# Kernel optimization log

Measured on AMD Instinct MI355X. Metric: run time of the kernel, lower is better.

## Reference

```python
import jax, jax.numpy as jnp
import numpy as np

D = 256      # embedding_dim
DI = 512     # inner dim = proj_factor * D
H = 4        # num heads
DH = DI // H # head dim
L = 4        # num blocks
K = 4        # causal conv kernel size

def _ln(x, g, b):
    mu = jnp.mean(x, -1, keepdims=True)
    v = jnp.var(x, -1, keepdims=True)
    return (x - mu) * jax.lax.rsqrt(v + 1e-5) * g + b

def _causal_conv(x, w, b):
    # x [B,S,DI], w [K,DI] depthwise causal conv
    S = x.shape[1]
    xp = jnp.pad(x, ((0, 0), (K - 1, 0), (0, 0)))
    out = b
    for j in range(K):
        out = out + xp[:, j:j + S, :] * w[j]
    return out

def _mlstm(q, k, v, ip, fp):
    # parallel stabilized mLSTM. q,k,v [B,S,H,DH]; ip,fp [B,S,H]
    q = q.transpose(0, 2, 1, 3)
    k = k.transpose(0, 2, 1, 3)
    v = v.transpose(0, 2, 1, 3)
    ip = ip.transpose(0, 2, 1)  # [B,H,S]
    fp = fp.transpose(0, 2, 1)
    lf = jax.nn.log_sigmoid(fp)                      # log forget gates
    Fc = jnp.cumsum(lf, axis=-1)
    Fc = jnp.concatenate([jnp.zeros_like(Fc[..., :1]), Fc], axis=-1)  # [B,H,S+1]
    logfg = Fc[..., 1:, None] - Fc[..., None, 1:]    # [B,H,S,S]: sum of log f over (s,t]
    S_len = q.shape[2]
    tri = jnp.tril(jnp.ones((S_len, S_len), dtype=bool))
    logD = jnp.where(tri, logfg + ip[..., None, :], jnp.float32(-1e30))
    m = jnp.max(logD, axis=-1, keepdims=True)        # stabilizer
    Dm = jnp.exp(logD - m)
    qk = jnp.einsum('bhtd,bhsd->bhts', q, k) * (DH ** -0.5)
    C = qk * Dm
    norm = jnp.maximum(jnp.abs(jnp.sum(C, axis=-1, keepdims=True)), jnp.exp(-m))
    h = jnp.einsum('bhts,bhsd->bhtd', C / (norm + 1e-6), v)
    return h.transpose(0, 2, 1, 3)

def _forward(x, time_features, Wp, bp, ln_g, ln_b, Wup, bup, conv_w, conv_b,
             Wq, Wk, Wv, Wif, bif, gn_g, gn_b, skip, Wdown, bdown,
             lnf_g, lnf_b, Wf, bf):
    B, S = x.shape
    xi = jnp.concatenate([x[..., None], time_features], axis=-1)  # [B,S,5]
    h = xi @ Wp + bp                                              # [B,S,D]
    for l in range(L):
        res = h
        hn = _ln(h, ln_g[l], ln_b[l])
        up = hn @ Wup[l] + bup[l]                 # [B,S,2*DI]
        xm, z = up[..., :DI], up[..., DI:]
        xc = jax.nn.silu(_causal_conv(xm, conv_w[l], conv_b[l]))
        q = (xc @ Wq[l]).reshape(B, S, H, DH)
        k = (xc @ Wk[l]).reshape(B, S, H, DH)
        v = (xm @ Wv[l]).reshape(B, S, H, DH)
        gi = jnp.concatenate([q.reshape(B, S, DI), k.reshape(B, S, DI), v.reshape(B, S, DI)], axis=-1)
        gates = gi @ Wif[l] + bif[l]              # [B,S,2H]
        ht = _mlstm(q, k, v, gates[..., :H], gates[..., H:])  # [B,S,H,DH]
        ht = _ln(ht, gn_g[l].reshape(H, DH), gn_b[l].reshape(H, DH)).reshape(B, S, DI)
        ht = ht + skip[l] * xc
        ht = ht * jax.nn.silu(z)
        h = res + ht @ Wdown[l] + bdown[l]
    h = _ln(h, lnf_g, lnf_b)
    return h[:, -1, :] @ Wf + bf                  # [B,1]

def setup_inputs():
    key = jax.random.key(0)
    ks = jax.random.split(key, 16)
    B, S = 8, 1024
    sd = jnp.float32(0.02)
    return {
        'x': jax.random.normal(ks[0], (B, S), jnp.float32),
        'time_features': jax.random.normal(ks[1], (B, S, 4), jnp.float32),
        'Wp': jax.random.normal(ks[2], (5, D)) * sd, 'bp': jnp.zeros((D,)),
        'ln_g': jnp.ones((L, D)), 'ln_b': jnp.zeros((L, D)),
        'Wup': jax.random.normal(ks[3], (L, D, 2 * DI)) * sd, 'bup': jnp.zeros((L, 2 * DI)),
        'conv_w': jax.random.normal(ks[4], (L, K, DI)) * sd, 'conv_b': jnp.zeros((L, DI)),
        'Wq': jax.random.normal(ks[5], (L, DI, DI)) * sd,
        'Wk': jax.random.normal(ks[6], (L, DI, DI)) * sd,
        'Wv': jax.random.normal(ks[7], (L, DI, DI)) * sd,
        'Wif': jax.random.normal(ks[8], (L, 3 * DI, 2 * H)) * sd, 'bif': jnp.zeros((L, 2 * H)),
        'gn_g': jnp.ones((L, DI)), 'gn_b': jnp.zeros((L, DI)),
        'skip': jnp.ones((L, DI)),
        'Wdown': jax.random.normal(ks[9], (L, DI, D)) * sd, 'bdown': jnp.zeros((L, D)),
        'lnf_g': jnp.ones((D,)), 'lnf_b': jnp.zeros((D,)),
        'Wf': jax.random.normal(ks[10], (D, 1)) * sd, 'bf': jnp.zeros((1,)),
    }

def reference(x, time_features, Wp, bp, ln_g, ln_b, Wup, bup, conv_w, conv_b,
              Wq, Wk, Wv, Wif, bif, gn_g, gn_b, skip, Wdown, bdown,
              lnf_g, lnf_b, Wf, bf):
    return _forward(x, time_features, Wp, bp, ln_g, ln_b, Wup, bup, conv_w, conv_b,
                    Wq, Wk, Wv, Wif, bif, gn_g, gn_b, skip, Wdown, bdown,
                    lnf_g, lnf_b, Wf, bf)
```

## Files before the change

### kernel.cpp

```cpp
#include <hip/hip_runtime.h>
#include <hip/hip_bf16.h>
#include <math.h>

#define S 1024
#define NLAYER 4

typedef __bf16 bf16x8 __attribute__((ext_vector_type(8)));
typedef float floatx4 __attribute__((ext_vector_type(4)));

__device__ __forceinline__ float wave_sum(float v) {
  #pragma unroll
  for (int off = 32; off > 0; off >>= 1) v += __shfl_xor(v, off, 64);
  return v;
}

__global__ __launch_bounds__(256) void embed_kernel(
    const float* __restrict__ x, const float* __restrict__ tf,
    const float* __restrict__ Wp, const float* __restrict__ bp,
    const float* __restrict__ g, const float* __restrict__ b,
    float* __restrict__ h, __bf16* __restrict__ hn) {
  int row = blockIdx.x;
  int n = threadIdx.x;
  float xv = x[row];
  const float* t4 = tf + (size_t)row * 4;
  float acc = bp[n] + xv * Wp[n];
  acc += t4[0] * Wp[256 + n];
  acc += t4[1] * Wp[512 + n];
  acc += t4[2] * Wp[768 + n];
  acc += t4[3] * Wp[1024 + n];
  h[(size_t)row * 256 + n] = acc;
  __shared__ float red[4];
  int wid = n >> 6, lane = n & 63;
  float s = wave_sum(acc);
  if (lane == 0) red[wid] = s;
  __syncthreads();
  float mu = (red[0] + red[1] + red[2] + red[3]) * (1.f / 256.f);
  __syncthreads();
  float d = acc - mu;
  float s2 = wave_sum(d * d);
  if (lane == 0) red[wid] = s2;
  __syncthreads();
  float var = (red[0] + red[1] + red[2] + red[3]) * (1.f / 256.f);
  float rs = rsqrtf(var + 1e-5f);
  hn[(size_t)row * 256 + n] = (__bf16)(d * rs * g[n] + b[n]);
}

__global__ __launch_bounds__(256) void wtrans_kernel(
    const float* __restrict__ Wup, const float* __restrict__ Wq,
    const float* __restrict__ Wk, const float* __restrict__ Wv,
    const float* __restrict__ Wdown,
    __bf16* __restrict__ WupT, __bf16* __restrict__ WqkT,
    __bf16* __restrict__ WvT, __bf16* __restrict__ WdownT) {
  __shared__ float T[32][33];
  int bid = blockIdx.x;
  int layer = bid / 1152, rr = bid % 1152;
  const float* src; __bf16* dst; int K, N, tile;
  if (rr < 256)       { src = Wup   + layer * 262144; dst = WupT  + layer * 262144;          K = 256; N = 1024; tile = rr; }
  else if (rr < 512)  { src = Wq    + layer * 262144; dst = WqkT  + layer * 524288;          K = 512; N = 512;  tile = rr - 256; }
  else if (rr < 768)  { src = Wk    + layer * 262144; dst = WqkT  + layer * 524288 + 262144; K = 512; N = 512;  tile = rr - 512; }
  else if (rr < 1024) { src = Wv    + layer * 262144; dst = WvT   + layer * 262144;          K = 512; N = 512;  tile = rr - 768; }
  else                { src = Wdown + layer * 131072; dst = WdownT + layer * 131072;         K = 512; N = 256;  tile = rr - 1024; }
  int ntn = N >> 5;
  int tk = tile / ntn, tn = tile % ntn;
  int tid = threadIdx.x;
  int r = tid >> 3, c4 = (tid & 7) * 4;
  float4 v = *(const float4*)(src + (size_t)(tk * 32 + r) * N + tn * 32 + c4);
  T[c4 + 0][r] = v.x; T[c4 + 1][r] = v.y; T[c4 + 2][r] = v.z; T[c4 + 3][r] = v.w;
  __syncthreads();
  __bf16 o[4];
  #pragma unroll
  for (int j = 0; j < 4; ++j) o[j] = (__bf16)T[r][c4 + j];
  *(uint2*)(dst + (size_t)(tn * 32 + r) * K + tk * 32 + c4) = *(uint2*)o;
}

__global__ __launch_bounds__(256) void wgprep_kernel(
    const float* __restrict__ Wq, const float* __restrict__ Wk,
    const float* __restrict__ Wv, const float* __restrict__ Wif,
    float* __restrict__ wg) {
  int bid = blockIdx.x;
  int l = bid >> 8;
  int rem = bid & 255;
  int sel = rem >> 7;
  int kg = rem & 127;
  int tid = threadIdx.x;
  int wv = tid >> 6, lane = tid & 63;
  int k = kg * 4 + wv;
  const float* wif = Wif + (size_t)l * 1536 * 8;
  float part[8] = {0, 0, 0, 0, 0, 0, 0, 0};
  if (sel == 0) {
    const float* qr = Wq + (size_t)l * 262144 + (size_t)k * 512;
    const float* kr = Wk + (size_t)l * 262144 + (size_t)k * 512;
    #pragma unroll
    for (int i = 0; i < 8; ++i) {
      int n = lane + i * 64;
      float qv = qr[n], kv = kr[n];
      const float* wq8 = wif + (size_t)n * 8;
      const float* wk8 = wif + (size_t)(512 + n) * 8;
      #pragma unroll
      for (int j = 0; j < 8; ++j) part[j] += qv * wq8[j] + kv * wk8[j];
    }
  } else {
    const float* vr = Wv + (size_t)l * 262144 + (size_t)k * 512;
    #pragma unroll
    for (int i = 0; i < 8; ++i) {
      int n = lane + i * 64;
      float vv = vr[n];
      const float* wv8 = wif + (size_t)(1024 + n) * 8;
      #pragma unroll
      for (int j = 0; j < 8; ++j) part[j] += vv * wv8[j];
    }
  }
  #pragma unroll
  for (int j = 0; j < 8; ++j) part[j] = wave_sum(part[j]);
  if (lane < 8) wg[(size_t)l * 8192 + sel * 4096 + (size_t)k * 8 + lane] = part[lane];
}

__global__ __launch_bounds__(256) void ln256_kernel(
    const float* __restrict__ x, const float* __restrict__ g,
    const float* __restrict__ b, __bf16* __restrict__ y) {
  int row = blockIdx.x, tid = threadIdx.x;
  __shared__ float red[4];
  float v = x[(size_t)row * 256 + tid];
  float s = wave_sum(v);
  int wid = tid >> 6, lane = tid & 63;
  if (lane == 0) red[wid] = s;
  __syncthreads();
  float mu = (red[0] + red[1] + red[2] + red[3]) * (1.f / 256.f);
  __syncthreads();
  float d = v - mu;
  float s2 = wave_sum(d * d);
  if (lane == 0) red[wid] = s2;
  __syncthreads();
  float var = (red[0] + red[1] + red[2] + red[3]) * (1.f / 256.f);
  float rs = rsqrtf(var + 1e-5f);
  y[(size_t)row * 256 + tid] = (__bf16)(d * rs * g[tid] + b[tid]);
}

template <int MODE, int ACC>
__global__ __launch_bounds__(256) void hgemm(
    const __bf16* __restrict__ A, int lda,
    const __bf16* __restrict__ BT, int Kdim,
    const float* __restrict__ bias,
    void* __restrict__ Cout, int ldc) {
  __shared__ __bf16 As[128][40];
  __shared__ __bf16 Bs[128][40];
  int tid = threadIdx.x;
  int bm = blockIdx.x * 128, bn = blockIdx.y * 128;
  int wid = tid >> 6, lane = tid & 63;
  int wr = wid >> 1, wc = wid & 1;
  int lg = lane >> 4, li = lane & 15;
  floatx4 acc[4][4];
  #pragma unroll
  for (int i = 0; i < 4; ++i)
    #pragma unroll
    for (int j = 0; j < 4; ++j) acc[i][j] = (floatx4)(0.f);

  int arow = tid >> 2, aseg = tid & 3;
  bf16x8 pa0, pa1, pb0, pb1;
  auto pre = [&](int k0) {
    pa0 = *(const bf16x8*)(A + (size_t)(bm + arow) * lda + k0 + aseg * 8);
    pa1 = *(const bf16x8*)(A + (size_t)(bm + arow + 64) * lda + k0 + aseg * 8);
    pb0 = *(const bf16x8*)(BT + (size_t)(bn + arow) * Kdim + k0 + aseg * 8);
    pb1 = *(const bf16x8*)(BT + (size_t)(bn + arow + 64) * Kdim + k0 + aseg * 8);
  };
  pre(0);
  for (int k0 = 0; k0 < Kdim; k0 += 32) {
    __syncthreads();
    *(bf16x8*)&As[arow][aseg * 8] = pa0;
    *(bf16x8*)&As[arow + 64][aseg * 8] = pa1;
    *(bf16x8*)&Bs[arow][aseg * 8] = pb0;
    *(bf16x8*)&Bs[arow + 64][aseg * 8] = pb1;
    __syncthreads();
    if (k0 + 32 < Kdim) pre(k0 + 32);
    bf16x8 af[4], bfr[4];
    #pragma unroll
    for (int mi = 0; mi < 4; ++mi)
      af[mi] = *(const bf16x8*)&As[wr * 64 + mi * 16 + li][lg * 8];
    #pragma unroll
    for (int ni = 0; ni < 4; ++ni)
      bfr[ni] = *(const bf16x8*)&Bs[wc * 64 + ni * 16 + li][lg * 8];
    #pragma unroll
    for (int mi = 0; mi < 4; ++mi)
      #pragma unroll
      for (int ni = 0; ni < 4; ++ni)
        acc[mi][ni] = __builtin_amdgcn_mfma_f32_16x16x32_bf16(af[mi], bfr[ni], acc[mi][ni], 0, 0, 0);
  }
  if (MODE == 1) {
    __bf16* eb = &As[0][0];
    const int PITCH = 136;
    __bf16* C = (__bf16*)Cout;
    #pragma unroll
    for (int mi = 0; mi < 4; ++mi) {
      __syncthreads();
      #pragma unroll
      for (int ni = 0; ni < 4; ++ni) {
        int col = wc * 64 + ni * 16 + li;
        float bz = bias ? bias[bn + col] : 0.f;
        #pragma unroll
        for (int r = 0; r < 4; ++r) {
          int lr = wr * 16 + lg * 4 + r;
          eb[lr * PITCH + col] = (__bf16)(acc[mi][ni][r] + bz);
        }
      }
      __syncthreads();
      #pragma unroll
      for (int i = 0; i < 2; ++i) {
        int lr = (tid >> 4) + i * 16;
        int c8 = (tid & 15) * 8;
        bf16x8 v = *(const bf16x8*)&eb[lr * PITCH + c8];
        int row_g = bm + (lr >> 4) * 64 + mi * 16 + (lr & 15);
        *(bf16x8*)(C + (size_t)row_g * ldc + bn + c8) = v;
      }
    }
  } else {
    #pragma unroll
    for (int mi = 0; mi < 4; ++mi) {
      int row = bm + wr * 64 + mi * 16 + lg * 4;
      #pragma unroll
      for (int ni = 0; ni < 4; ++ni) {
        int col = bn + wc * 64 + ni * 16 + li;
        if (MODE == 2) {
          __bf16 o4[4];
          #pragma unroll
          for (int r = 0; r < 4; ++r) o4[r] = (__bf16)acc[mi][ni][r];
          __bf16* vt = (__bf16*)Cout;
          size_t off = ((size_t)((row >> 10) * 4 + (col >> 7)) * 128 + (col & 127)) * 1024 + (row & 1023);
          *(uint2*)(vt + off) = *(uint2*)o4;
        } else {
          float bz = bias ? bias[col] : 0.f;
          float* C = (float*)Cout;
          #pragma unroll
          for (int r = 0; r < 4; ++r) {
            float v = acc[mi][ni][r] + bz;
            if (ACC) v += C[(size_t)(row + r) * ldc + col];
            C[(size_t)(row + r) * ldc + col] = v;
          }
        }
      }
    }
  }
}

__global__ __launch_bounds__(256) void conv_silu_kernel(
    const __bf16* __restrict__ up, const float* __restrict__ cw,
    const float* __restrict__ cb, const float* __restrict__ wg,
    const float* __restrict__ bif, __bf16* __restrict__ xc,
    float* __restrict__ gates) {
  int tid = threadIdx.x;
  int wv = tid >> 6, lane = tid & 63;
  int row = blockIdx.x * 4 + wv;
  int c8 = lane * 8;
  int t = row & (S - 1);
  float acc[8];
  *(float4*)&acc[0] = *(const float4*)(cb + c8);
  *(float4*)&acc[4] = *(const float4*)(cb + c8 + 4);
  float xm[8];
  #pragma unroll
  for (int j = 0; j < 4; ++j) {
    int tt = t - 3 + j;
    if (tt >= 0) {
      bf16x8 xv = *(const bf16x8*)(up + (size_t)(row - 3 + j) * 1024 + c8);
      float4 w0 = *(const float4*)(cw + j * 512 + c8);
      float4 w1 = *(const float4*)(cw + j * 512 + c8 + 4);
      acc[0] += w0.x * (float)xv[0]; acc[1] += w0.y * (float)xv[1];
      acc[2] += w0.z * (float)xv[2]; acc[3] += w0.w * (float)xv[3];
      acc[4] += w1.x * (float)xv[4]; acc[5] += w1.y * (float)xv[5];
      acc[6] += w1.z * (float)xv[6]; acc[7] += w1.w * (float)xv[7];
      if (j == 3) {
        #pragma unroll
        for (int m = 0; m < 8; ++m) xm[m] = (float)xv[m];
      }
    }
  }
  bf16x8 o;
  float xcs[8];
  #pragma unroll
  for (int m = 0; m < 8; ++m) {
    float sg = 1.f / (1.f + __expf(-acc[m]));
    xcs[m] = acc[m] * sg;
    o[m] = (__bf16)xcs[m];
  }
  *(bf16x8*)(xc + (size_t)row * 512 + c8) = o;
  const float* w1 = wg + (size_t)c8 * 8;
  const float* w2 = wg + 4096 + (size_t)c8 * 8;
  float part[8] = {0, 0, 0, 0, 0, 0, 0, 0};
  #pragma unroll
  for (int m = 0; m < 8; ++m) {
    const float* a = w1 + m * 8;
    const float* b = w2 + m * 8;
    #pragma unroll
    for (int j = 0; j < 8; ++j) part[j] += xcs[m] * a[j] + xm[m] * b[j];
  }
  #pragma unroll
  for (int j = 0; j < 8; ++j) part[j] = wave_sum(part[j]);
  if (lane < 8) gates[(size_t)row * 8 + lane] = part[lane] + bif[lane];
}

__global__ __launch_bounds__(64) void scan_kernel(
    const float* __restrict__ gates, float* __restrict__ gout,
    float* __restrict__ Mout, float* __restrict__ NFout) {
  int bh = blockIdx.x;
  int bb = bh >> 2, hh = bh & 3;
  int lane = threadIdx.x;
  float ip[16], pf[16];
  #pragma unroll
  for (int i = 0; i < 16; ++i) {
    int t = lane * 16 + i;
    const float* grow = gates + ((size_t)(bb * S + t)) * 8;
    ip[i] = grow[hh];
    float fp = grow[4 + hh];
    float lf = fminf(fp, 0.f) - log1pf(__expf(-fabsf(fp)));
    pf[i] = (i == 0) ? lf : pf[i - 1] + lf;
  }
  float T = pf[15];
  float inc = T;
  #pragma unroll
  for (int off = 1; off < 64; off <<= 1) {
    float v = __shfl_up(inc, off, 64);
    if (lane >= off) inc += v;
  }
  float excl = inc - T;
  float F[16], g[16], pm[16];
  #pragma unroll
  for (int i = 0; i < 16; ++i) {
    F[i] = excl + pf[i];
    g[i] = ip[i] - F[i];
    pm[i] = (i == 0) ? g[0] : fmaxf(pm[i - 1], g[i]);
  }
  float Mx = pm[15];
  float incm = Mx;
  #pragma unroll
  for (int off = 1; off < 64; off <<= 1) {
    float v = __shfl_up(incm, off, 64);
    if (lane >= off) incm = fmaxf(incm, v);
  }
  float em = __shfl_up(incm, 1, 64);
  if (lane == 0) em = -3.4e38f;
  #pragma unroll
  for (int i = 0; i < 16; ++i) {
    int t = lane * 16 + i;
    size_t o = (size_t)bh * S + t;
    float M = fmaxf(em, pm[i]);
    gout[o] = g[i];
    Mout[o] = M;
    NFout[o] = __expf(-F[i] - M);
  }
}

__global__ __launch_bounds__(256, 1) void attn_kernel(
    const __bf16* __restrict__ qk, const __bf16* __restrict__ vT,
    const float* __restrict__ gbuf, const float* __restrict__ Mbuf,
    const float* __restrict__ NFbuf,
    const float* __restrict__ gn_g, const float* __restrict__ gn_b,
    const float* __restrict__ skip,
    const __bf16* __restrict__ xc, const __bf16* __restrict__ up,
    __bf16* __restrict__ hd) {
  __shared__ __bf16 Ks[64][136];
  __shared__ __bf16 Vs[128][72];
  __shared__ __bf16 plds[4][2][16][72];
  __shared__ float gls[64];
  __shared__ float glds[128], blds[128], slds[128];
  int px = blockIdx.y, bh = blockIdx.x;
  int tqA = px, tqB = 15 - px;
  int bb = bh >> 2, hh = bh & 3;
  int tid = threadIdx.x;
  int wv = tid >> 6, lane = tid & 63;
  int lg = lane >> 4, li = lane & 15;
  int tbA = tqA * 64 + wv * 16;
  int tbB = tqB * 64 + wv * 16;
  const float scale = 0.08838834764831845f;

  if (tid < 128) {
    glds[tid] = gn_g[hh * 128 + tid];
    blds[tid] = gn_b[hh * 128 + tid];
    slds[tid] = skip[hh * 128 + tid];
  }

  bf16x8 aqA[4], aqB[4];
  {
    const __bf16* qpA = qk + ((size_t)(bb * S + tbA + li)) * 1024 + hh * 128 + lg * 8;
    const __bf16* qpB = qk + ((size_t)(bb * S + tbB + li)) * 1024 + hh * 128 + lg * 8;
    #pragma unroll
    for (int cd = 0; cd < 4; ++cd) {
      aqA[cd] = *(const bf16x8*)(qpA + cd * 32);
      aqB[cd] = *(const bf16x8*)(qpB + cd * 32);
    }
  }
  float mlA[4], nfA[4], mlB[4], nfB[4];
  #pragma unroll
  for (int r = 0; r < 4; ++r) {
    mlA[r] = Mbuf[(size_t)bh * S + tbA + lg * 4 + r];
    nfA[r] = NFbuf[(size_t)bh * S + tbA + lg * 4 + r];
    mlB[r] = Mbuf[(size_t)bh * S + tbB + lg * 4 + r];
    nfB[r] = NFbuf[(size_t)bh * S + tbB + lg * 4 + r];
  }

  floatx4 oA[8], oB[8];
  #pragma unroll
  for (int df = 0; df < 8; ++df) { oA[df] = (floatx4)(0.f); oB[df] = (floatx4)(0.f); }
  float rsA[4] = {0, 0, 0, 0}, rsB[4] = {0, 0, 0, 0};

  int krow = tid >> 3, kcol = tid & 7;
  bf16x8 kreg[4], vreg[4];
  float greg = 0.f;
  auto preload = [&](int st) {
    int s0 = st * 64;
    const __bf16* kp = qk + ((size_t)(bb * S + s0 + krow)) * 1024 + 512 + hh * 128;
    kreg[0] = *(const bf16x8*)(kp + kcol * 8);
    kreg[1] = *(const bf16x8*)(kp + (size_t)32 * 1024 + kcol * 8);
    kreg[2] = *(const bf16x8*)(kp + 64 + kcol * 8);
    kreg[3] = *(const bf16x8*)(kp + (size_t)32 * 1024 + 64 + kcol * 8);
    #pragma unroll
    for (int i = 0; i < 4; ++i)
      vreg[i] = *(const bf16x8*)(vT + ((size_t)(bh * 128 + krow + i * 32)) * 1024 + s0 + kcol * 8);
    if (tid < 64) greg = gbuf[(size_t)bh * S + s0 + tid];
  };
  preload(0);

  for (int st = 0; st <= tqB; ++st) {
    __syncthreads();
    *(bf16x8*)&Ks[krow][kcol * 8] = kreg[0];
    *(bf16x8*)&Ks[krow + 32][kcol * 8] = kreg[1];
    *(bf16x8*)&Ks[krow][64 + kcol * 8] = kreg[2];
    *(bf16x8*)&Ks[krow + 32][64 + kcol * 8] = kreg[3];
    #pragma unroll
    for (int i = 0; i < 4; ++i) *(bf16x8*)&Vs[krow + i * 32][kcol * 8] = vreg[i];
    if (tid < 64) gls[tid] = greg;
    __syncthreads();
    if (st < tqB) preload(st + 1);

    int s0 = st * 64;
    bool actA = (st <= tqA);
    #pragma unroll
    for (int ns = 0; ns < 4; ++ns) {
      bf16x8 bk0 = *(const bf16x8*)&Ks[ns * 16 + li][lg * 8];
      bf16x8 bk1 = *(const bf16x8*)&Ks[ns * 16 + li][32 + lg * 8];
      bf16x8 bk2 = *(const bf16x8*)&Ks[ns * 16 + li][64 + lg * 8];
      bf16x8 bk3 = *(const bf16x8*)&Ks[ns * 16 + li][96 + lg * 8];
      int s = s0 + ns * 16 + li;
      float gv = gls[ns * 16 + li];
      if (actA) {
        floatx4 pa = (floatx4)(0.f);
        pa = __builtin_amdgcn_mfma_f32_16x16x32_bf16(aqA[0], bk0, pa, 0, 0, 0);
        pa = __builtin_amdgcn_mfma_f32_16x16x32_bf16(aqA[1], bk1, pa, 0, 0, 0);
        pa = __builtin_amdgcn_mfma_f32_16x16x32_bf16(aqA[2], bk2, pa, 0, 0, 0);
        pa = __builtin_amdgcn_mfma_f32_16x16x32_bf16(aqA[3], bk3, pa, 0, 0, 0);
        #pragma unroll
        for (int r = 0; r < 4; ++r) {
          int t = tbA + lg * 4 + r;
          float val = pa[r] * scale * __expf(gv - mlA[r]);
          float w = (s <= t) ? val : 0.f;
          rsA[r] += w;
          plds[wv][0][lg * 4 + r][ns * 16 + li] = (__bf16)w;
        }
      }
      {
        floatx4 pb = (floatx4)(0.f);
        pb = __builtin_amdgcn_mfma_f32_16x16x32_bf16(aqB[0], bk0, pb, 0, 0, 0);
        pb = __builtin_amdgcn_mfma_f32_16x16x32_bf16(aqB[1], bk1, pb, 0, 0, 0);
        pb = __builtin_amdgcn_mfma_f32_16x16x32_bf16(aqB[2], bk2, pb, 0, 0, 0);
        pb = __builtin_amdgcn_mfma_f32_16x16x32_bf16(aqB[3], bk3, pb, 0, 0, 0);
        #pragma unroll
        for (int r = 0; r < 4; ++r) {
          int t = tbB + lg * 4 + r;
          float val = pb[r] * scale * __expf(gv - mlB[r]);
          float w = (s <= t) ? val : 0.f;
          rsB[r] += w;
          plds[wv][1][lg * 4 + r][ns * 16 + li] = (__bf16)w;
        }
      }
    }
    bf16x8 apA0, apA1, apB0, apB1;
    if (actA) {
      apA0 = *(const bf16x8*)&plds[wv][0][li][lg * 8];
      apA1 = *(const bf16x8*)&plds[wv][0][li][32 + lg * 8];
    }
    apB0 = *(const bf16x8*)&plds[wv][1][li][lg * 8];
    apB1 = *(const bf16x8*)&plds[wv][1][li][32 + lg * 8];
    #pragma unroll
    for (int df = 0; df < 8; ++df) {
      bf16x8 bv0 = *(const bf16x8*)&Vs[df * 16 + li][lg * 8];
      bf16x8 bv1 = *(const bf16x8*)&Vs[df * 16 + li][32 + lg * 8];
      if (actA) {
        oA[df] = __builtin_amdgcn_mfma_f32_16x16x32_bf16(apA0, bv0, oA[df], 0, 0, 0);
        oA[df] = __builtin_amdgcn_mfma_f32_16x16x32_bf16(apA1, bv1, oA[df], 0, 0, 0);
      }
      oB[df] = __builtin_amdgcn_mfma_f32_16x16x32_bf16(apB0, bv0, oB[df], 0, 0, 0);
      oB[df] = __builtin_amdgcn_mfma_f32_16x16x32_bf16(apB1, bv1, oB[df], 0, 0, 0);
    }
  }
  #pragma unroll
  for (int r = 0; r < 4; ++r) {
    float a = rsA[r], b = rsB[r];
    a += __shfl_xor(a, 1, 64); a += __shfl_xor(a, 2, 64);
    a += __shfl_xor(a, 4, 64); a += __shfl_xor(a, 8, 64);
    b += __shfl_xor(b, 1, 64); b += __shfl_xor(b, 2, 64);
    b += __shfl_xor(b, 4, 64); b += __shfl_xor(b, 8, 64);
    rsA[r] = a; rsB[r] = b;
  }
  #pragma unroll
  for (int tile = 0; tile < 2; ++tile) {
    int tb = tile == 0 ? tbA : tbB;
    #pragma unroll
    for (int r = 0; r < 4; ++r) {
      float rs = tile == 0 ? rsA[r] : rsB[r];
      float nf = tile == 0 ? nfA[r] : nfB[r];
      float inv = 1.f / (fmaxf(fabsf(rs), nf) + 1e-6f);
      float v8[8], s1 = 0.f, s2 = 0.f;
      #pragma unroll
      for (int df = 0; df < 8; ++df) {
        float v = (tile == 0 ? oA[df][r] : oB[df][r]) * inv;
        v8[df] = v;
        s1 += v;
        s2 += v * v;
      }
      s1 += __shfl_xor(s1, 1, 64); s1 += __shfl_xor(s1, 2, 64);
      s1 += __shfl_xor(s1, 4, 64); s1 += __shfl_xor(s1, 8, 64);
      s2 += __shfl_xor(s2, 1, 64); s2 += __shfl_xor(s2, 2, 64);
      s2 += __shfl_xor(s2, 4, 64); s2 += __shfl_xor(s2, 8, 64);
      float mu = s1 * (1.f / 128.f);
      float var = s2 * (1.f / 128.f) - mu * mu;
      float rq = rsqrtf(var + 1e-5f);
      int t = tb + lg * 4 + r;
      const __bf16* xr = xc + ((size_t)(bb * S + t)) * 512 + hh * 128 + li;
      const __bf16* zr = up + ((size_t)(bb * S + t)) * 1024 + 512 + hh * 128 + li;
      __bf16* od = hd + ((size_t)(bb * S + t)) * 512 + hh * 128 + li;
      #pragma unroll
      for (int df = 0; df < 8; ++df) {
        int c = df * 16 + li;
        float ln = (v8[df] - mu) * rq * glds[c] + blds[c];
        float val = ln + slds[c] * (float)xr[df * 16];
        float z = (float)zr[df * 16];
        float sg = 1.f / (1.f + __expf(-z));
        od[df * 16] = (__bf16)(val * (z * sg));
      }
    }
  }
}

__global__ __launch_bounds__(256) void final_kernel(
    const float* __restrict__ h, const float* __restrict__ g,
    const float* __restrict__ b, const float* __restrict__ Wf,
    const float* __restrict__ bf, float* __restrict__ out) {
  int bb = blockIdx.x, tid = threadIdx.x;
  size_t row = (size_t)(bb * S + S - 1) * 256;
  __shared__ float red[4];
  float v = h[row + tid];
  float s = wave_sum(v);
  int wid = tid >> 6, lane = tid & 63;
  if (lane == 0) red[wid] = s;
  __syncthreads();
  float mu = (red[0] + red[1] + red[2] + red[3]) * (1.f / 256.f);
  __syncthreads();
  float d = v - mu;
  float s2 = wave_sum(d * d);
  if (lane == 0) red[wid] = s2;
  __syncthreads();
  float var = (red[0] + red[1] + red[2] + red[3]) * (1.f / 256.f);
  float rs = rsqrtf(var + 1e-5f);
  float ln = d * rs * g[tid] + b[tid];
  float p = ln * Wf[tid];
  float psum = wave_sum(p);
  __syncthreads();
  if (lane == 0) red[wid] = psum;
  __syncthreads();
  if (tid == 0) out[bb] = red[0] + red[1] + red[2] + red[3] + bf[0];
}

extern "C" void kernel_launch(void* const* d_in, const int* in_sizes, int n_in,
                              void* d_out, int out_size, void* d_ws, size_t ws_size,
                              hipStream_t stream) {
  const float* x      = (const float*)d_in[0];
  const float* tf     = (const float*)d_in[1];
  const float* Wp     = (const float*)d_in[2];
  const float* bp     = (const float*)d_in[3];
  const float* ln_g   = (const float*)d_in[4];
  const float* ln_b   = (const float*)d_in[5];
  const float* Wup    = (const float*)d_in[6];
  const float* bup    = (const float*)d_in[7];
  const float* conv_w = (const float*)d_in[8];
  const float* conv_b = (const float*)d_in[9];
  const float* Wq     = (const float*)d_in[10];
  const float* Wk     = (const float*)d_in[11];
  const float* Wv     = (const float*)d_in[12];
  const float* Wif    = (const float*)d_in[13];
  const float* bif    = (const float*)d_in[14];
  const float* gn_g   = (const float*)d_in[15];
  const float* gn_b   = (const float*)d_in[16];
  const float* skip   = (const float*)d_in[17];
  const float* Wdown  = (const float*)d_in[18];
  const float* bdown  = (const float*)d_in[19];
  const float* lnf_g  = (const float*)d_in[20];
  const float* lnf_b  = (const float*)d_in[21];
  const float* Wf     = (const float*)d_in[22];
  const float* bf     = (const float*)d_in[23];
  float* out = (float*)d_out;

  float* h     = (float*)d_ws;
  float* gates = h + 2097152;
  float* gbuf  = gates + 65536;
  float* Mbuf  = gbuf + 32768;
  float* NFbuf = Mbuf + 32768;
  float* wgbuf = NFbuf + 32768;
  __bf16* hn   = (__bf16*)(wgbuf + 32768);
  __bf16* up   = hn + 2097152;
  __bf16* xc   = up + 8388608;
  __bf16* qk   = xc + 4194304;
  __bf16* vT   = qk + 8388608;
  __bf16* hd   = vT + 4194304;
  __bf16* WupT   = hd + 4194304;
  __bf16* WqkT   = WupT + 1048576;
  __bf16* WvT    = WqkT + 2097152;
  __bf16* WdownT = WvT + 1048576;

  wtrans_kernel<<<4608, 256, 0, stream>>>(Wup, Wq, Wk, Wv, Wdown,
                                          WupT, WqkT, WvT, WdownT);
  wgprep_kernel<<<1024, 256, 0, stream>>>(Wq, Wk, Wv, Wif, wgbuf);
  embed_kernel<<<8192, 256, 0, stream>>>(x, tf, Wp, bp, ln_g, ln_b, h, hn);
  for (int l = 0; l < NLAYER; ++l) {
    if (l > 0)
      ln256_kernel<<<8192, 256, 0, stream>>>(h, ln_g + l * 256, ln_b + l * 256, hn);
    hgemm<1, 0><<<dim3(64, 8), 256, 0, stream>>>(
        hn, 256, WupT + (size_t)l * 262144, 256, bup + l * 1024, up, 1024);
    conv_silu_kernel<<<2048, 256, 0, stream>>>(up, conv_w + l * 2048, conv_b + l * 512,
                                               wgbuf + l * 8192, bif + l * 8, xc, gates);
    scan_kernel<<<32, 64, 0, stream>>>(gates, gbuf, Mbuf, NFbuf);
    hgemm<1, 0><<<dim3(64, 8), 256, 0, stream>>>(
        xc, 512, WqkT + (size_t)l * 524288, 512, nullptr, qk, 1024);
    hgemm<2, 0><<<dim3(64, 4), 256, 0, stream>>>(
        up, 1024, WvT + (size_t)l * 262144, 512, nullptr, vT, 0);
    attn_kernel<<<dim3(32, 8), 256, 0, stream>>>(
        qk, vT, gbuf, Mbuf, NFbuf, gn_g + l * 512, gn_b + l * 512, skip + l * 512,
        xc, up, hd);
    hgemm<0, 1><<<dim3(64, 2), 256, 0, stream>>>(
        hd, 512, WdownT + (size_t)l * 131072, 512, bdown + l * 256, h, 256);
  }
  final_kernel<<<8, 256, 0, stream>>>(h, lnf_g, lnf_b, Wf, bf, out);
}
```

Measured before the change: 728.4 us.

## Merge prep kernels, fuse QK and V GEMMs, add 64-row GEMM tiles

Combines the weight-transpose, gate-weight prep and embedding kernels into one launch. Fuses the QK and V projection GEMMs into a single grid, with the V part using 64-row tiles. Switches the down-projection GEMM to 64-row tiles so it launches 256 blocks instead of 128. The intent is to cut launch overhead and raise occupancy on the small GEMMs, at the cost of less reuse per tile and branchy blocks inside one grid.

```diff
diff --git a/kernel.cpp b/kernel.cpp
--- a/kernel.cpp
+++ b/kernel.cpp
@@ -14,12 +14,73 @@
   return v;
 }
 
-__global__ __launch_bounds__(256) void embed_kernel(
-    const float* __restrict__ x, const float* __restrict__ tf,
-    const float* __restrict__ Wp, const float* __restrict__ bp,
-    const float* __restrict__ g, const float* __restrict__ b,
-    float* __restrict__ h, __bf16* __restrict__ hn) {
-  int row = blockIdx.x;
+__device__ __forceinline__ void wtrans_body(
+    int bid, const float* Wup, const float* Wq, const float* Wk, const float* Wv,
+    const float* Wdown, __bf16* WupT, __bf16* WqkT, __bf16* WvT, __bf16* WdownT) {
+  __shared__ float T[32][33];
+  int layer = bid / 1152, rr = bid % 1152;
+  const float* src; __bf16* dst; int K, N, tile;
+  if (rr < 256)       { src = Wup   + layer * 262144; dst = WupT  + layer * 262144;          K = 256; N = 1024; tile = rr; }
+  else if (rr < 512)  { src = Wq    + layer * 262144; dst = WqkT  + layer * 524288;          K = 512; N = 512;  tile = rr - 256; }
+  else if (rr < 768)  { src = Wk    + layer * 262144; dst = WqkT  + layer * 524288 + 262144; K = 512; N = 512;  tile = rr - 512; }
+  else if (rr < 1024) { src = Wv    + layer * 262144; dst = WvT   + layer * 262144;          K = 512; N = 512;  tile = rr - 768; }
+  else                { src = Wdown + layer * 131072; dst = WdownT + layer * 131072;         K = 512; N = 256;  tile = rr - 1024; }
+  int ntn = N >> 5;
+  int tk = tile / ntn, tn = tile % ntn;
+  int tid = threadIdx.x;
+  int r = tid >> 3, c4 = (tid & 7) * 4;
+  float4 v = *(const float4*)(src + (size_t)(tk * 32 + r) * N + tn * 32 + c4);
+  T[c4 + 0][r] = v.x; T[c4 + 1][r] = v.y; T[c4 + 2][r] = v.z; T[c4 + 3][r] = v.w;
+  __syncthreads();
+  __bf16 o[4];
+  #pragma unroll
+  for (int j = 0; j < 4; ++j) o[j] = (__bf16)T[r][c4 + j];
+  *(uint2*)(dst + (size_t)(tn * 32 + r) * K + tk * 32 + c4) = *(uint2*)o;
+}
+
+__device__ __forceinline__ void wgprep_body(
+    int bid, const float* Wq, const float* Wk, const float* Wv,
+    const float* Wif, float* wg) {
+  int l = bid >> 8;
+  int rem = bid & 255;
+  int sel = rem >> 7;
+  int kg = rem & 127;
+  int tid = threadIdx.x;
+  int wv = tid >> 6, lane = tid & 63;
+  int k = kg * 4 + wv;
+  const float* wif = Wif + (size_t)l * 1536 * 8;
+  float part[8] = {0, 0, 0, 0, 0, 0, 0, 0};
+  if (sel == 0) {
+    const float* qr = Wq + (size_t)l * 262144 + (size_t)k * 512;
+    const float* kr = Wk + (size_t)l * 262144 + (size_t)k * 512;
+    #pragma unroll
+    for (int i = 0; i < 8; ++i) {
+      int n = lane + i * 64;
+      float qv = qr[n], kv = kr[n];
+      const float* wq8 = wif + (size_t)n * 8;
+      const float* wk8 = wif + (size_t)(512 + n) * 8;
+      #pragma unroll
+      for (int j = 0; j < 8; ++j) part[j] += qv * wq8[j] + kv * wk8[j];
+    }
+  } else {
+    const float* vr = Wv + (size_t)l * 262144 + (size_t)k * 512;
+    #pragma unroll
+    for (int i = 0; i < 8; ++i) {
+      int n = lane + i * 64;
+      float vv = vr[n];
+      const float* wv8 = wif + (size_t)(1024 + n) * 8;
+      #pragma unroll
+      for (int j = 0; j < 8; ++j) part[j] += vv * wv8[j];
+    }
+  }
+  #pragma unroll
+  for (int j = 0; j < 8; ++j) part[j] = wave_sum(part[j]);
+  if (lane < 8) wg[(size_t)l * 8192 + sel * 4096 + (size_t)k * 8 + lane] = part[lane];
+}
+
+__device__ __forceinline__ void embed_body(
+    int row, const float* x, const float* tf, const float* Wp, const float* bp,
+    const float* g, const float* b, float* h, __bf16* hn) {
   int n = threadIdx.x;
   float xv = x[row];
   const float* t4 = tf + (size_t)row * 4;
@@ -45,74 +106,24 @@
   hn[(size_t)row * 256 + n] = (__bf16)(d * rs * g[n] + b[n]);
 }
 
-__global__ __launch_bounds__(256) void wtrans_kernel(
+__global__ __launch_bounds__(256) void prep_kernel(
+    const float* __restrict__ x, const float* __restrict__ tf,
+    const float* __restrict__ Wp, const float* __restrict__ bp,
+    const float* __restrict__ ln_g, const float* __restrict__ ln_b,
     const float* __restrict__ Wup, const float* __restrict__ Wq,
     const float* __restrict__ Wk, const float* __restrict__ Wv,
-    const float* __restrict__ Wdown,
+    const float* __restrict__ Wdown, const float* __restrict__ Wif,
     __bf16* __restrict__ WupT, __bf16* __restrict__ WqkT,
-    __bf16* __restrict__ WvT, __bf16* __restrict__ WdownT) {
-  __shared__ float T[32][33];
+    __bf16* __restrict__ WvT, __bf16* __restrict__ WdownT,
+    float* __restrict__ wg, float* __restrict__ h, __bf16* __restrict__ hn) {
   int bid = blockIdx.x;
-  int layer = bid / 1152, rr = bid % 1152;
-  const float* src; __bf16* dst; int K, N, tile;
-  if (rr < 256)       { src = Wup   + layer * 262144; dst = WupT  + layer * 262144;          K = 256; N = 1024; tile = rr; }
-  else if (rr < 512)  { src = Wq    + layer * 262144; dst = WqkT  + layer * 524288;          K = 512; N = 512;  tile = rr - 256; }
-  else if (rr < 768)  { src = Wk    + layer * 262144; dst = WqkT  + layer * 524288 + 262144; K = 512; N = 512;  tile = rr - 512; }
-  else if (rr < 1024) { src = Wv    + layer * 262144; dst = WvT   + layer * 262144;          K = 512; N = 512;  tile = rr - 768; }
-  else                { src = Wdown + layer * 131072; dst = WdownT + layer * 131072;         K = 512; N = 256;  tile = rr - 1024; }
-  int ntn = N >> 5;
-  int tk = tile / ntn, tn = tile % ntn;
-  int tid = threadIdx.x;
-  int r = tid >> 3, c4 = (tid & 7) * 4;
-  float4 v = *(const float4*)(src + (size_t)(tk * 32 + r) * N + tn * 32 + c4);
-  T[c4 + 0][r] = v.x; T[c4 + 1][r] = v.y; T[c4 + 2][r] = v.z; T[c4 + 3][r] = v.w;
-  __syncthreads();
-  __bf16 o[4];
-  #pragma unroll
-  for (int j = 0; j < 4; ++j) o[j] = (__bf16)T[r][c4 + j];
-  *(uint2*)(dst + (size_t)(tn * 32 + r) * K + tk * 32 + c4) = *(uint2*)o;
-}
-
-__global__ __launch_bounds__(256) void wgprep_kernel(
-    const float* __restrict__ Wq, const float* __restrict__ Wk,
-    const float* __restrict__ Wv, const float* __restrict__ Wif,
-    float* __restrict__ wg) {
-  int bid = blockIdx.x;
-  int l = bid >> 8;
-  int rem = bid & 255;
-  int sel = rem >> 7;
-  int kg = rem & 127;
-  int tid = threadIdx.x;
-  int wv = tid >> 6, lane = tid & 63;
-  int k = kg * 4 + wv;
-  const float* wif = Wif + (size_t)l * 1536 * 8;
-  float part[8] = {0, 0, 0, 0, 0, 0, 0, 0};
-  if (sel == 0) {
-    const float* qr = Wq + (size_t)l * 262144 + (size_t)k * 512;
-    const float* kr = Wk + (size_t)l * 262144 + (size_t)k * 512;
-    #pragma unroll
-    for (int i = 0; i < 8; ++i) {
-      int n = lane + i * 64;
-      float qv = qr[n], kv = kr[n];
-      const float* wq8 = wif + (size_t)n * 8;
-      const float* wk8 = wif + (size_t)(512 + n) * 8;
-      #pragma unroll
-      for (int j = 0; j < 8; ++j) part[j] += qv * wq8[j] + kv * wk8[j];
-    }
+  if (bid < 4608) {
+    wtrans_body(bid, Wup, Wq, Wk, Wv, Wdown, WupT, WqkT, WvT, WdownT);
+  } else if (bid < 4608 + 1024) {
+    wgprep_body(bid - 4608, Wq, Wk, Wv, Wif, wg);
   } else {
-    const float* vr = Wv + (size_t)l * 262144 + (size_t)k * 512;
-    #pragma unroll
-    for (int i = 0; i < 8; ++i) {
-      int n = lane + i * 64;
-      float vv = vr[n];
-      const float* wv8 = wif + (size_t)(1024 + n) * 8;
-      #pragma unroll
-      for (int j = 0; j < 8; ++j) part[j] += vv * wv8[j];
-    }
-  }
-  #pragma unroll
-  for (int j = 0; j < 8; ++j) part[j] = wave_sum(part[j]);
-  if (lane < 8) wg[(size_t)l * 8192 + sel * 4096 + (size_t)k * 8 + lane] = part[lane];
+    embed_body(bid - 5632, x, tf, Wp, bp, ln_g, ln_b, h, hn);
+  }
 }
 
 __global__ __launch_bounds__(256) void ln256_kernel(
@@ -136,22 +147,25 @@
   y[(size_t)row * 256 + tid] = (__bf16)(d * rs * g[tid] + b[tid]);
 }
 
-template <int MODE, int ACC>
-__global__ __launch_bounds__(256) void hgemm(
+template <int TM, int MODE, int ACC>
+__device__ __forceinline__ void hgemm_body(
+    char* smem_raw,
     const __bf16* __restrict__ A, int lda,
     const __bf16* __restrict__ BT, int Kdim,
     const float* __restrict__ bias,
-    void* __restrict__ Cout, int ldc) {
-  __shared__ __bf16 As[128][40];
-  __shared__ __bf16 Bs[128][40];
+    void* __restrict__ Cout, int ldc, int bxi, int byi) {
+  auto As = (__bf16(*)[40])smem_raw;
+  auto Bs = (__bf16(*)[40])(smem_raw + (size_t)TM * 80);
   int tid = threadIdx.x;
-  int bm = blockIdx.x * 128, bn = blockIdx.y * 128;
+  int bm = bxi * TM, bn = byi * 128;
   int wid = tid >> 6, lane = tid & 63;
   int wr = wid >> 1, wc = wid & 1;
   int lg = lane >> 4, li = lane & 15;
-  floatx4 acc[4][4];
-  #pragma unroll
-  for (int i = 0; i < 4; ++i)
+  constexpr int MI = TM / 32;
+  constexpr int WROW = TM / 2;
+  floatx4 acc[MI][4];
+  #pragma unroll
+  for (int i = 0; i < MI; ++i)
     #pragma unroll
     for (int j = 0; j < 4; ++j) acc[i][j] = (floatx4)(0.f);
 
@@ -159,38 +173,43 @@
   bf16x8 pa0, pa1, pb0, pb1;
   auto pre = [&](int k0) {
     pa0 = *(const bf16x8*)(A + (size_t)(bm + arow) * lda + k0 + aseg * 8);
-    pa1 = *(const bf16x8*)(A + (size_t)(bm + arow + 64) * lda + k0 + aseg * 8);
+    if constexpr (TM == 128)
+      pa1 = *(const bf16x8*)(A + (size_t)(bm + arow + 64) * lda + k0 + aseg * 8);
     pb0 = *(const bf16x8*)(BT + (size_t)(bn + arow) * Kdim + k0 + aseg * 8);
     pb1 = *(const bf16x8*)(BT + (size_t)(bn + arow + 64) * Kdim + k0 + aseg * 8);
   };
   pre(0);
   for (int k0 = 0; k0 < Kdim; k0 += 32) {
     __syncthreads();
-    *(bf16x8*)&As[arow][aseg * 8] = pa0;
-    *(bf16x8*)&As[arow + 64][aseg * 8] = pa1;
+    if constexpr (TM == 128) {
+      *(bf16x8*)&As[arow][aseg * 8] = pa0;
+      *(bf16x8*)&As[arow + 64][aseg * 8] = pa1;
+    } else {
+      *(bf16x8*)&As[arow][aseg * 8] = pa0;
+    }
     *(bf16x8*)&Bs[arow][aseg * 8] = pb0;
     *(bf16x8*)&Bs[arow + 64][aseg * 8] = pb1;
     __syncthreads();
     if (k0 + 32 < Kdim) pre(k0 + 32);
-    bf16x8 af[4], bfr[4];
-    #pragma unroll
-    for (int mi = 0; mi < 4; ++mi)
-      af[mi] = *(const bf16x8*)&As[wr * 64 + mi * 16 + li][lg * 8];
+    bf16x8 af[MI], bfr[4];
+    #pragma unroll
+    for (int mi = 0; mi < MI; ++mi)
+      af[mi] = *(const bf16x8*)&As[wr * WROW + mi * 16 + li][lg * 8];
     #pragma unroll
     for (int ni = 0; ni < 4; ++ni)
       bfr[ni] = *(const bf16x8*)&Bs[wc * 64 + ni * 16 + li][lg * 8];
     #pragma unroll
-    for (int mi = 0; mi < 4; ++mi)
+    for (int mi = 0; mi < MI; ++mi)
       #pragma unroll
       for (int ni = 0; ni < 4; ++ni)
         acc[mi][ni] = __builtin_amdgcn_mfma_f32_16x16x32_bf16(af[mi], bfr[ni], acc[mi][ni], 0, 0, 0);
   }
-  if (MODE == 1) {
-    __bf16* eb = &As[0][0];
+  if constexpr (MODE == 1) {
+    __bf16* eb = (__bf16*)smem_raw;
     const int PITCH = 136;
     __bf16* C = (__bf16*)Cout;
     #pragma unroll
-    for (int mi = 0; mi < 4; ++mi) {
+    for (int mi = 0; mi < MI; ++mi) {
       __syncthreads();
       #pragma unroll
       for (int ni = 0; ni < 4; ++ni) {
@@ -214,12 +233,12 @@
     }
   } else {
     #pragma unroll
-    for (int mi = 0; mi < 4; ++mi) {
-      int row = bm + wr * 64 + mi * 16 + lg * 4;
+    for (int mi = 0; mi < MI; ++mi) {
+      int row = bm + wr * WROW + mi * 16 + lg * 4;
       #pragma unroll
       for (int ni = 0; ni < 4; ++ni) {
         int col = bn + wc * 64 + ni * 16 + li;
-        if (MODE == 2) {
+        if constexpr (MODE == 2) {
           __bf16 o4[4];
           #pragma unroll
           for (int r = 0; r < 4; ++r) o4[r] = (__bf16)acc[mi][ni][r];
@@ -238,6 +257,32 @@
         }
       }
     }
+  }
+}
+
+template <int TM, int MODE, int ACC>
+__global__ __launch_bounds__(256) void hgemm(
+    const __bf16* __restrict__ A, int lda,
+    const __bf16* __restrict__ BT, int Kdim,
+    const float* __restrict__ bias,
+    void* __restrict__ Cout, int ldc) {
+  extern __shared__ char smem[];
+  hgemm_body<TM, MODE, ACC>(smem, A, lda, BT, Kdim, bias, Cout, ldc,
+                            blockIdx.x, blockIdx.y);
+}
+
+__global__ __launch_bounds__(256) void qkv_kernel(
+    const __bf16* __restrict__ xc, const __bf16* __restrict__ WqkT,
+    __bf16* __restrict__ qk, const __bf16* __restrict__ up,
+    const __bf16* __restrict__ WvT, __bf16* __restrict__ vT) {
+  extern __shared__ char smem[];
+  if (blockIdx.y < 8) {
+    hgemm_body<128, 1, 0>(smem, xc, 512, WqkT, 512, nullptr, qk, 1024,
+                          blockIdx.x, blockIdx.y);
+  } else {
+    int j = blockIdx.y - 8;
+    hgemm_body<64, 2, 0>(smem, up, 1024, WvT, 512, nullptr, vT, 0,
+                         blockIdx.x * 2 + (j & 1), j >> 1);
   }
 }
 
@@ -613,26 +658,23 @@
   __bf16* WvT    = WqkT + 2097152;
   __bf16* WdownT = WvT + 1048576;
 
-  wtrans_kernel<<<4608, 256, 0, stream>>>(Wup, Wq, Wk, Wv, Wdown,
-                                          WupT, WqkT, WvT, WdownT);
-  wgprep_kernel<<<1024, 256, 0, stream>>>(Wq, Wk, Wv, Wif, wgbuf);
-  embed_kernel<<<8192, 256, 0, stream>>>(x, tf, Wp, bp, ln_g, ln_b, h, hn);
+  prep_kernel<<<13824, 256, 0, stream>>>(
+      x, tf, Wp, bp, ln_g, ln_b, Wup, Wq, Wk, Wv, Wdown, Wif,
+      WupT, WqkT, WvT, WdownT, wgbuf, h, hn);
   for (int l = 0; l < NLAYER; ++l) {
     if (l > 0)
       ln256_kernel<<<8192, 256, 0, stream>>>(h, ln_g + l * 256, ln_b + l * 256, hn);
-    hgemm<1, 0><<<dim3(64, 8), 256, 0, stream>>>(
+    hgemm<128, 1, 0><<<dim3(64, 8), 256, 20480, stream>>>(
         hn, 256, WupT + (size_t)l * 262144, 256, bup + l * 1024, up, 1024);
     conv_silu_kernel<<<2048, 256, 0, stream>>>(up, conv_w + l * 2048, conv_b + l * 512,
                                                wgbuf + l * 8192, bif + l * 8, xc, gates);
     scan_kernel<<<32, 64, 0, stream>>>(gates, gbuf, Mbuf, NFbuf);
-    hgemm<1, 0><<<dim3(64, 8), 256, 0, stream>>>(
-        xc, 512, WqkT + (size_t)l * 524288, 512, nullptr, qk, 1024);
-    hgemm<2, 0><<<dim3(64, 4), 256, 0, stream>>>(
-        up, 1024, WvT + (size_t)l * 262144, 512, nullptr, vT, 0);
+    qkv_kernel<<<dim3(64, 16), 256, 20480, stream>>>(
+        xc, WqkT + (size_t)l * 524288, qk, up, WvT + (size_t)l * 262144, vT);
     attn_kernel<<<dim3(32, 8), 256, 0, stream>>>(
         qk, vT, gbuf, Mbuf, NFbuf, gn_g + l * 512, gn_b + l * 512, skip + l * 512,
         xc, up, hd);
-    hgemm<0, 1><<<dim3(64, 2), 256, 0, stream>>>(
+    hgemm<64, 0, 1><<<dim3(128, 2), 256, 15360, stream>>>(
         hd, 512, WdownT + (size_t)l * 131072, 512, bdown + l * 256, h, 256);
   }
   final_kernel<<<8, 256, 0, stream>>>(h, lnf_g, lnf_b, Wf, bf, out);
```

New measurement: 674.1 us. -7.5%, faster.
